# Optimization experiments

Hardware: AMD Instinct MI355X
Metric: run time of the kernel (lower is better)

Reference implementation:

```python
import jax, jax.numpy as jnp
import numpy as np

NUM_HEADS = 8
EPS = 1e-9


def setup_inputs() -> dict:
    key = jax.random.key(0)
    ks = jax.random.split(key, 5)
    B, S, D = 2, 2048, 512
    x = jax.random.normal(ks[0], (B, S, D), dtype=jnp.float32)
    Wq = jax.random.normal(ks[1], (D, D), dtype=jnp.float32) * (1.0 / np.sqrt(D))
    Wk = jax.random.normal(ks[2], (D, D), dtype=jnp.float32) * (1.0 / np.sqrt(D))
    Wv = jax.random.normal(ks[3], (D, D), dtype=jnp.float32) * (1.0 / np.sqrt(D))
    Wo = jax.random.normal(ks[4], (D, D), dtype=jnp.float32) * (1.0 / np.sqrt(D))
    gamma = jnp.ones((D,), dtype=jnp.float32)
    beta = jnp.zeros((D,), dtype=jnp.float32)
    return {"x": x, "Wq": Wq, "Wk": Wk, "Wv": Wv, "Wo": Wo, "gamma": gamma, "beta": beta}


def _layernorm(x, gamma, beta):
    mean = jnp.mean(x, axis=-1, keepdims=True)
    var = jnp.mean(jnp.square(x - mean), axis=-1, keepdims=True)
    return gamma * ((x - mean) * jax.lax.rsqrt(var + EPS)) + beta


def reference(x, Wq, Wk, Wv, Wo, gamma, beta):
    B, S, D = x.shape
    H = NUM_HEADS
    dh = D // H
    # Note: in the original, K_V=(inputs, inputs) is captured BEFORE LayerNorm,
    # so only Q is layer-normalized; K and V use the raw inputs.
    q_in = _layernorm(x, gamma, beta)
    Q = jnp.einsum('bsd,de->bse', q_in, Wq).reshape(B, S, H, dh)
    K = jnp.einsum('bsd,de->bse', x, Wk).reshape(B, S, H, dh)
    V = jnp.einsum('bsd,de->bse', x, Wv).reshape(B, S, H, dh)
    # scaled dot-product attention (bias = 0, dropout disabled since dropout=1)
    scores = jnp.einsum('bqhd,bkhd->bhqk', Q, K) / jnp.sqrt(jnp.float32(dh))
    attn = jax.nn.softmax(scores, axis=-1)
    ctx = jnp.einsum('bhqk,bkhd->bqhd', attn, V).reshape(B, S, D)
    out = jnp.einsum('bsd,de->bse', ctx, Wo) + x  # output proj + residual
    return out
```

## Files before the change

kernel.cpp:

```cpp
#include <hip/hip_runtime.h>

typedef __bf16 bf16x8 __attribute__((ext_vector_type(8)));
typedef float f32x4 __attribute__((ext_vector_type(4)));

#define SCALE_LOG2E 0.18033688011112042f

__device__ __forceinline__ float bf2f(unsigned int u) { return __uint_as_float(u << 16); }
__device__ __forceinline__ unsigned short f2bfu(float f) {
    union { __bf16 h; unsigned short u; } v;
    v.h = (__bf16)f;
    return v.u;
}
__device__ __forceinline__ unsigned int pk2bf(float a, float b) {
    union { __bf16 h[2]; unsigned int u; } v;
    v.h[0] = (__bf16)a; v.h[1] = (__bf16)b;
    return v.u;
}

__device__ int probe_bf16(const void* xp) {
    const unsigned short* u = (const unsigned short*)xp;
    int cnt = 0;
    for (int i = 0; i < 128; i++) {
        unsigned e = (u[i] >> 7) & 0xFFu;
        cnt += (e == 0u || (e >= 0x6Cu && e <= 0x8Au)) ? 1 : 0;
    }
    return cnt >= 120;
}

__global__ __launch_bounds__(64)
void probe_k(const void* __restrict__ x, const void* __restrict__ Wq, int* __restrict__ flags) {
    if (threadIdx.x == 0) {
        flags[0] = probe_bf16(x);
        flags[1] = probe_bf16(Wq);
    }
}

__device__ __forceinline__ void load8f(const void* p, int isb, size_t idx, float* o) {
    if (isb) {
        uint4 v = *(const uint4*)((const unsigned short*)p + idx);
        o[0] = bf2f(v.x & 0xffffu); o[1] = bf2f(v.x >> 16);
        o[2] = bf2f(v.y & 0xffffu); o[3] = bf2f(v.y >> 16);
        o[4] = bf2f(v.z & 0xffffu); o[5] = bf2f(v.z >> 16);
        o[6] = bf2f(v.w & 0xffffu); o[7] = bf2f(v.w >> 16);
    } else {
        const float* f = (const float*)p + idx;
        float4 a = *(const float4*)f;
        float4 b = *(const float4*)(f + 4);
        o[0] = a.x; o[1] = a.y; o[2] = a.z; o[3] = a.w;
        o[4] = b.x; o[5] = b.y; o[6] = b.z; o[7] = b.w;
    }
}
__device__ __forceinline__ void load2f(const void* p, int isb, size_t idx, float& a, float& b) {
    if (isb) {
        unsigned int v = *(const unsigned int*)((const unsigned short*)p + idx);
        a = bf2f(v & 0xffffu); b = bf2f(v >> 16);
    } else {
        float2 f = *(const float2*)((const float*)p + idx);
        a = f.x; b = f.y;
    }
}
__device__ __forceinline__ float load1f(const void* p, int isb, size_t idx) {
    return isb ? bf2f((unsigned int)((const unsigned short*)p)[idx]) : ((const float*)p)[idx];
}

__global__ __launch_bounds__(256)
void setup_k(const void* __restrict__ x, const void* __restrict__ Wq, const void* __restrict__ Wk,
             const void* __restrict__ Wv, const void* __restrict__ Wo,
             const void* __restrict__ gamma, const void* __restrict__ beta,
             float* __restrict__ rowstats, float* __restrict__ gf, float* __restrict__ bfv,
             unsigned short* __restrict__ WT, const int* __restrict__ flags) {
    const int t = threadIdx.x;
    const int bid = blockIdx.x;
    if (bid < 1024) {
        const int isb = flags[1];
        __shared__ float tile[32][33];
        const int which = bid >> 8, tl = bid & 255;
        const int bx = (tl & 15) * 32, by = (tl >> 4) * 32;
        const void* W = (which == 0) ? Wq : (which == 1) ? Wk : (which == 2) ? Wv : Wo;
        unsigned short* dst = WT + (size_t)which * 512 * 512;
        const int xx = t & 31, y0 = t >> 5;
#pragma unroll
        for (int i = 0; i < 4; i++) {
            int y = y0 + i * 8;
            tile[y][xx] = load1f(W, isb, (size_t)(by + y) * 512 + bx + xx);
        }
        __syncthreads();
#pragma unroll
        for (int i = 0; i < 4; i++) {
            int y = y0 + i * 8;
            dst[(size_t)(bx + y) * 512 + by + xx] = f2bfu(tile[xx][y]);
        }
        return;
    }
    const int isb = flags[0];
    if (bid >= 5120) {
        const void* src = (bid == 5120) ? gamma : beta;
        float* dst = (bid == 5120) ? gf : bfv;
        float a, b;
        load2f(src, isb, (size_t)t * 2, a, b);
        dst[t * 2] = a; dst[t * 2 + 1] = b;
        return;
    }
    const int row = bid - 1024;
    float a, b;
    load2f(x, isb, (size_t)row * 512 + t * 2, a, b);
    float s = a + b, sq = a * a + b * b;
#pragma unroll
    for (int msk = 1; msk < 64; msk <<= 1) {
        s += __shfl_xor(s, msk);
        sq += __shfl_xor(sq, msk);
    }
    __shared__ float red[8];
    if ((t & 63) == 0) { red[t >> 6] = s; red[4 + (t >> 6)] = sq; }
    __syncthreads();
    if (t == 0) {
        float S = red[0] + red[1] + red[2] + red[3];
        float SQ = red[4] + red[5] + red[6] + red[7];
        float mean = S * (1.0f / 512.0f);
        float var = SQ * (1.0f / 512.0f) - mean * mean;
        rowstats[2 * row] = mean;
        rowstats[2 * row + 1] = rsqrtf(fmaxf(var, 0.0f) + 1e-9f);
    }
}

__global__ __launch_bounds__(512)
void proj_all_k(const void* __restrict__ x, const unsigned short* __restrict__ WT,
                const float* __restrict__ rowstats, const float* __restrict__ gf,
                const float* __restrict__ bfv, unsigned short* __restrict__ Qb,
                unsigned short* __restrict__ Kb, unsigned short* __restrict__ VtF,
                const int* __restrict__ flags) {
    __shared__ unsigned short As[128 * 40];
    __shared__ unsigned short Bs[128 * 40];
    __shared__ float Gs[512], Bts[512];
    const int t = threadIdx.x;
    const int isb = flags[0];
    const int w = t >> 6, lane = t & 63;
    const int quad = lane >> 4, ln = lane & 15;
    const f32x4 zero = {0.f, 0.f, 0.f, 0.f};

    if (blockIdx.z == 0) {
        const int role = blockIdx.x & 1;
        const int n0 = (blockIdx.x >> 1) * 128;
        const int m0 = blockIdx.y * 128;
        const unsigned short* BT = WT + (size_t)role * 512 * 512;
        unsigned short* out = role ? Kb : Qb;
        const int wm = w & 1, wn = w >> 1;
        Gs[t] = gf[t]; Bts[t] = bfv[t];

        f32x4 acc[4][2];
#pragma unroll
        for (int i = 0; i < 4; i++)
#pragma unroll
            for (int j = 0; j < 2; j++) acc[i][j] = zero;

        for (int kt = 0; kt < 512; kt += 32) {
            __syncthreads();
            {
                int r = t >> 2, c8 = t & 3;
                size_t gidx = (size_t)(m0 + r) * 512 + kt + c8 * 8;
                if (isb && role == 1) {
                    *(uint4*)(&As[r * 40 + c8 * 8]) = *(const uint4*)((const unsigned short*)x + gidx);
                } else {
                    float f[8];
                    load8f(x, isb, gidx, f);
                    if (role == 0) {
                        float mean = rowstats[2 * (m0 + r)];
                        float inv = rowstats[2 * (m0 + r) + 1];
#pragma unroll
                        for (int j = 0; j < 8; j++) {
                            int k = kt + c8 * 8 + j;
                            f[j] = (f[j] - mean) * inv * Gs[k] + Bts[k];
                        }
                    }
                    unsigned int pk[4];
#pragma unroll
                    for (int j = 0; j < 4; j++) pk[j] = pk2bf(f[2 * j], f[2 * j + 1]);
                    *(uint4*)(&As[r * 40 + c8 * 8]) = make_uint4(pk[0], pk[1], pk[2], pk[3]);
                }
            }
            {
                int r = t >> 2, c8 = t & 3;
                *(uint4*)(&Bs[r * 40 + c8 * 8]) = *(const uint4*)(BT + (size_t)(n0 + r) * 512 + kt + c8 * 8);
            }
            __syncthreads();
            bf16x8 af[4], bfr[2];
#pragma unroll
            for (int i = 0; i < 4; i++)
                af[i] = *(const bf16x8*)(&As[(wm * 64 + i * 16 + ln) * 40 + quad * 8]);
#pragma unroll
            for (int j = 0; j < 2; j++)
                bfr[j] = *(const bf16x8*)(&Bs[(wn * 32 + j * 16 + ln) * 40 + quad * 8]);
#pragma unroll
            for (int i = 0; i < 4; i++)
#pragma unroll
                for (int j = 0; j < 2; j++)
                    acc[i][j] = __builtin_amdgcn_mfma_f32_16x16x32_bf16(af[i], bfr[j], acc[i][j], 0, 0, 0);
        }
#pragma unroll
        for (int i = 0; i < 4; i++)
#pragma unroll
            for (int j = 0; j < 2; j++)
#pragma unroll
                for (int r = 0; r < 4; r++) {
                    int grow = m0 + wm * 64 + i * 16 + quad * 4 + r;
                    int gcol = n0 + wn * 32 + j * 16 + ln;
                    float v = acc[i][j][r];
                    if (role == 0) v *= SCALE_LOG2E;
                    out[(size_t)grow * 512 + gcol] = f2bfu(v);
                }
    } else {
        const int m0 = blockIdx.x * 64;
        const int n0 = blockIdx.y * 128;
        const unsigned short* AW = WT + (size_t)2 * 512 * 512;
        const int wv = w & 3, wn2 = w >> 2;

        f32x4 acc[4];
#pragma unroll
        for (int j = 0; j < 4; j++) acc[j] = zero;

        for (int kt = 0; kt < 512; kt += 32) {
            __syncthreads();
            if (t < 256) {
                int r = t >> 2, c8 = t & 3;
                *(uint4*)(&As[r * 40 + c8 * 8]) = *(const uint4*)(AW + (size_t)(m0 + r) * 512 + kt + c8 * 8);
            }
            {
                int r = t >> 2, c8 = t & 3;
                size_t gidx = (size_t)(n0 + r) * 512 + kt + c8 * 8;
                if (isb) {
                    *(uint4*)(&Bs[r * 40 + c8 * 8]) = *(const uint4*)((const unsigned short*)x + gidx);
                } else {
                    float f[8];
                    load8f(x, isb, gidx, f);
                    unsigned int pk[4];
#pragma unroll
                    for (int j = 0; j < 4; j++) pk[j] = pk2bf(f[2 * j], f[2 * j + 1]);
                    *(uint4*)(&Bs[r * 40 + c8 * 8]) = make_uint4(pk[0], pk[1], pk[2], pk[3]);
                }
            }
            __syncthreads();
            bf16x8 af = *(const bf16x8*)(&As[(wv * 16 + ln) * 40 + quad * 8]);
#pragma unroll
            for (int j = 0; j < 4; j++) {
                bf16x8 bfr = *(const bf16x8*)(&Bs[(wn2 * 64 + j * 16 + ln) * 40 + quad * 8]);
                acc[j] = __builtin_amdgcn_mfma_f32_16x16x32_bf16(af, bfr, acc[j], 0, 0, 0);
            }
        }
#pragma unroll
        for (int j = 0; j < 4; j++)
#pragma unroll
            for (int r = 0; r < 4; r++) {
                int grow = m0 + wv * 16 + quad * 4 + r;
                int gcol = n0 + wn2 * 64 + j * 16 + ln;
                VtF[(size_t)grow * 4096 + gcol] = f2bfu(acc[j][r]);
            }
    }
}

__global__ __launch_bounds__(1024, 1)
void attn_m_k(const unsigned short* __restrict__ Qb, const unsigned short* __restrict__ Kb,
              const unsigned short* __restrict__ VtF, unsigned short* __restrict__ ctx) {
    const int S = 2048, PT = 72, NT = 32;
    const int t = threadIdx.x;
    const int qb = blockIdx.x, h = blockIdx.y, b = blockIdx.z;
    const int w = t >> 6, lane = t & 63;
    const int quad = lane >> 4, ln = lane & 15;
    const int kq = w & 3, qh = w >> 2;

    __shared__ unsigned short sh[27648];
    unsigned short* const KsA = sh;
    unsigned short* const KsB = sh + 4608;
    unsigned short* const Vt0 = sh + 9216;
    unsigned short* const Vt1 = sh + 13824;
    unsigned short* const Vt2 = sh + 18432;
    unsigned short* const Vt3 = sh + 23040;
    unsigned short* const Qs  = sh + 18432;

    const size_t baseQ  = (size_t)(b * S + qb * 128) * 512 + h * 64;
    const size_t baseK  = (size_t)(b * S) * 512 + h * 64;
    const size_t baseVt = (size_t)(h * 64) * 4096 + (size_t)b * S;

    const int c8 = t & 7;
    const int r64 = (t & 511) >> 3;
    const int stoff = r64 * PT + c8 * 8;

    const int kfo0 = (kq * 16 + ln) * PT + quad * 8;
    const int vto  = ln * PT + kq * 16 + quad * 4;

    const unsigned short* const gK = Kb + baseK + (size_t)r64 * 512 + c8 * 8;
    const unsigned short* const gV = VtF + baseVt + (size_t)r64 * 4096 + c8 * 8;

    uint4 sa, sb;
    if (t < 512) { sa = *(const uint4*)(gK); sb = *(const uint4*)(gK + 32768); }
    else         { sa = *(const uint4*)(gV); sb = *(const uint4*)(gV + 64); }

    {
        const int rQ = t >> 3;
        *(uint4*)(&Qs[rQ * PT + c8 * 8]) = *(const uint4*)(Qb + baseQ + (size_t)rQ * 512 + c8 * 8);
    }
    __syncthreads();
    bf16x8 qf[2][2];
#pragma unroll
    for (int s2 = 0; s2 < 2; s2++)
#pragma unroll
        for (int i = 0; i < 2; i++)
            qf[s2][i] = *(const bf16x8*)(&Qs[(qh * 32 + s2 * 16 + ln) * PT + quad * 8 + 32 * i]);

    f32x4 acc[2][4];
    const f32x4 zero = {0.f, 0.f, 0.f, 0.f};
#pragma unroll
    for (int s2 = 0; s2 < 2; s2++)
#pragma unroll
        for (int j = 0; j < 4; j++) acc[s2][j] = zero;
    float lsum0 = 0.f, lsum1 = 0.f;

#define STAGE(KS, VT, R)                                                    \
    {                                                                       \
        if (t < 512) *(uint4*)(&KS[stoff]) = R;                             \
        else         *(uint4*)(&VT[stoff]) = R;                             \
    }
#define PRELOAD(R, kt)                                                      \
    if ((kt) < NT) {                                                        \
        if (t < 512) R = *(const uint4*)(gK + (size_t)(kt) * 32768);        \
        else         R = *(const uint4*)(gV + (size_t)(kt) * 64);           \
    }
#define QK_EXP(KS, U00, U01, U10, U11)                                      \
    {                                                                       \
        bf16x8 kf0 = *(const bf16x8*)(&KS[kfo0]);                           \
        bf16x8 kf1 = *(const bf16x8*)(&KS[kfo0 + 32]);                      \
        f32x4 sc0 = zero, sc1 = zero;                                       \
        sc0 = __builtin_amdgcn_mfma_f32_16x16x32_bf16(kf0, qf[0][0], sc0, 0, 0, 0); \
        sc0 = __builtin_amdgcn_mfma_f32_16x16x32_bf16(kf1, qf[0][1], sc0, 0, 0, 0); \
        sc1 = __builtin_amdgcn_mfma_f32_16x16x32_bf16(kf0, qf[1][0], sc1, 0, 0, 0); \
        sc1 = __builtin_amdgcn_mfma_f32_16x16x32_bf16(kf1, qf[1][1], sc1, 0, 0, 0); \
        float a0 = __builtin_amdgcn_exp2f(fminf(sc0[0], 30.f));             \
        float a1 = __builtin_amdgcn_exp2f(fminf(sc0[1], 30.f));             \
        float a2 = __builtin_amdgcn_exp2f(fminf(sc0[2], 30.f));             \
        float a3 = __builtin_amdgcn_exp2f(fminf(sc0[3], 30.f));             \
        lsum0 += (a0 + a1) + (a2 + a3);                                     \
        U00 = pk2bf(a0, a1); U01 = pk2bf(a2, a3);                           \
        float b0 = __builtin_amdgcn_exp2f(fminf(sc1[0], 30.f));             \
        float b1 = __builtin_amdgcn_exp2f(fminf(sc1[1], 30.f));             \
        float b2 = __builtin_amdgcn_exp2f(fminf(sc1[2], 30.f));             \
        float b3 = __builtin_amdgcn_exp2f(fminf(sc1[3], 30.f));             \
        lsum1 += (b0 + b1) + (b2 + b3);                                     \
        U10 = pk2bf(b0, b1); U11 = pk2bf(b2, b3);                           \
    }
#define PV4(VTE, VTO)                                                       \
    {                                                                       \
        bf16x8 ap0 = __builtin_bit_cast(bf16x8, make_uint4(uA00, uA01, uB00, uB01)); \
        bf16x8 ap1 = __builtin_bit_cast(bf16x8, make_uint4(uA10, uA11, uB10, uB11)); \
        _Pragma("unroll")                                                   \
        for (int nt = 0; nt < 4; nt++) {                                    \
            uint2 ve = *(const uint2*)(&VTE[vto + nt * 16 * PT]);           \
            uint2 vo = *(const uint2*)(&VTO[vto + nt * 16 * PT]);           \
            bf16x8 vb = __builtin_bit_cast(bf16x8, make_uint4(ve.x, ve.y, vo.x, vo.y)); \
            acc[0][nt] = __builtin_amdgcn_mfma_f32_16x16x32_bf16(ap0, vb, acc[0][nt], 0, 0, 0); \
            acc[1][nt] = __builtin_amdgcn_mfma_f32_16x16x32_bf16(ap1, vb, acc[1][nt], 0, 0, 0); \
        }                                                                   \
    }

    for (int m = 0; m < 8; m++) {
        const int T = m * 4;
        unsigned int uA00, uA01, uA10, uA11, uB00, uB01, uB10, uB11;
        STAGE(KsA, Vt0, sa);
        __syncthreads();
        PRELOAD(sa, T + 2);
        QK_EXP(KsA, uA00, uA01, uA10, uA11);
        STAGE(KsB, Vt1, sb);
        __syncthreads();
        PRELOAD(sb, T + 3);
        QK_EXP(KsB, uB00, uB01, uB10, uB11);
        PV4(Vt0, Vt1);
        STAGE(KsA, Vt2, sa);
        __syncthreads();
        PRELOAD(sa, T + 4);
        QK_EXP(KsA, uA00, uA01, uA10, uA11);
        STAGE(KsB, Vt3, sb);
        __syncthreads();
        PRELOAD(sb, T + 5);
        QK_EXP(KsB, uB00, uB01, uB10, uB11);
        PV4(Vt2, Vt3);
    }
#undef STAGE
#undef PRELOAD
#undef QK_EXP
#undef PV4

    lsum0 += __shfl_xor(lsum0, 16);
    lsum0 += __shfl_xor(lsum0, 32);
    lsum1 += __shfl_xor(lsum1, 16);
    lsum1 += __shfl_xor(lsum1, 32);

    __syncthreads();
    float* scr  = (float*)sh;
    float* lred = scr + 13056;
    if (quad == 0) {
        lred[kq * 128 + qh * 32 + ln] = lsum0;
        lred[kq * 128 + qh * 32 + 16 + ln] = lsum1;
    }
#pragma unroll
    for (int rr = 0; rr < 2; rr++) {
        __syncthreads();
        if ((qh >> 1) == rr && kq != 0) {
            const int pb = (kq - 1) * 4352 + ((qh & 1) * 32 + quad * 4) * 68 + ln;
#pragma unroll
            for (int s2 = 0; s2 < 2; s2++)
#pragma unroll
                for (int nt = 0; nt < 4; nt++)
#pragma unroll
                    for (int r = 0; r < 4; r++)
                        scr[pb + (s2 * 16 + r) * 68 + nt * 16] = acc[s2][nt][r];
        }
        __syncthreads();
        if ((qh >> 1) == rr && kq == 0) {
#pragma unroll
            for (int s2 = 0; s2 < 2; s2++) {
                const size_t baseO = (size_t)(b * S + qb * 128 + qh * 32 + s2 * 16 + quad * 4) * 512 + h * 64 + ln;
#pragma unroll
                for (int r = 0; r < 4; r++) {
                    int qrow = qh * 32 + s2 * 16 + quad * 4 + r;
                    float lt = lred[qrow] + lred[128 + qrow] + lred[256 + qrow] + lred[384 + qrow];
                    float inv = 1.0f / lt;
                    int rb = ((qh & 1) * 32 + s2 * 16 + quad * 4 + r) * 68 + ln;
#pragma unroll
                    for (int nt = 0; nt < 4; nt++) {
                        float v = acc[s2][nt][r] + scr[rb + nt * 16] + scr[4352 + rb + nt * 16] + scr[8704 + rb + nt * 16];
                        ctx[baseO + (size_t)r * 512 + nt * 16] = f2bfu(v * inv);
                    }
                }
            }
        }
    }
}

__global__ __launch_bounds__(512)
void outproj_k(const unsigned short* __restrict__ ctx, const unsigned short* __restrict__ BT,
               const void* __restrict__ x, void* __restrict__ outp, const int* __restrict__ flags) {
    __shared__ unsigned short As[128 * 40];
    __shared__ unsigned short Bs[64 * 40];
    const int t = threadIdx.x;
    const int isb = flags[0];
    const int m0 = blockIdx.y * 128, n0 = blockIdx.x * 64;
    const int w = t >> 6, lane = t & 63;
    const int wm = w & 1, wn = w >> 1;
    const int quad = lane >> 4, ln = lane & 15;

    f32x4 acc[4];
    const f32x4 zero = {0.f, 0.f, 0.f, 0.f};
#pragma unroll
    for (int i = 0; i < 4; i++) acc[i] = zero;

    for (int kt = 0; kt < 512; kt += 32) {
        __syncthreads();
        {
            int r = t >> 2, c8 = t & 3;
            *(uint4*)(&As[r * 40 + c8 * 8]) = *(const uint4*)(ctx + (size_t)(m0 + r) * 512 + kt + c8 * 8);
        }
        if (t < 256) {
            int r = t >> 2, c8 = t & 3;
            *(uint4*)(&Bs[r * 40 + c8 * 8]) = *(const uint4*)(BT + (size_t)(n0 + r) * 512 + kt + c8 * 8);
        }
        __syncthreads();
        bf16x8 af[4];
#pragma unroll
        for (int i = 0; i < 4; i++)
            af[i] = *(const bf16x8*)(&As[(wm * 64 + i * 16 + ln) * 40 + quad * 8]);
        bf16x8 bfr = *(const bf16x8*)(&Bs[(wn * 16 + ln) * 40 + quad * 8]);
#pragma unroll
        for (int i = 0; i < 4; i++)
            acc[i] = __builtin_amdgcn_mfma_f32_16x16x32_bf16(af[i], bfr, acc[i], 0, 0, 0);
    }
#pragma unroll
    for (int i = 0; i < 4; i++)
#pragma unroll
        for (int r = 0; r < 4; r++) {
            int grow = m0 + wm * 64 + i * 16 + quad * 4 + r;
            int gcol = n0 + wn * 16 + ln;
            size_t idx = (size_t)grow * 512 + gcol;
            float v = acc[i][r] + load1f(x, isb, idx);
            if (isb) ((unsigned short*)outp)[idx] = f2bfu(v);
            else     ((float*)outp)[idx] = v;
        }
}

__global__ __launch_bounds__(256)
void fill_k(unsigned short* out, int n) {
    int i = blockIdx.x * 256 + threadIdx.x;
    if (i < n) out[i] = 0x4442;
}

extern "C" void kernel_launch(void* const* d_in, const int* in_sizes, int n_in,
                              void* d_out, int out_size, void* d_ws, size_t ws_size,
                              hipStream_t stream) {
    const void* x     = d_in[0];
    const void* Wq    = d_in[1];
    const void* Wk    = d_in[2];
    const void* Wv    = d_in[3];
    const void* Wo    = d_in[4];
    const void* gamma = d_in[5];
    const void* beta  = d_in[6];

    const size_t NW = 512 * 512;
    const size_t NX = 4096 * 512;
    char* w = (char*)d_ws;

    const size_t FULL_STATS_OFF = 2097152 + 3 * NX * 2;
    const size_t NEED_FULL = FULL_STATS_OFF + 32768 + 4096 + 16;

    if (ws_size < NEED_FULL) {
        fill_k<<<(out_size + 255) / 256, 256, 0, stream>>>((unsigned short*)d_out, out_size);
        return;
    }

    unsigned short* WT  = (unsigned short*)w;
    unsigned short* Qb  = (unsigned short*)(w + 2097152);
    unsigned short* Kb  = Qb + NX;
    unsigned short* VtF = Kb + NX;
    unsigned short* ctx = Qb;
    float* rowstats = (float*)(w + FULL_STATS_OFF);
    float* gf = rowstats + 8192;
    float* bfv = gf + 512;
    int* flags = (int*)(bfv + 512);

    probe_k<<<1, 64, 0, stream>>>(x, Wq, flags);
    setup_k<<<5122, 256, 0, stream>>>(x, Wq, Wk, Wv, Wo, gamma, beta, rowstats, gf, bfv, WT, flags);
    proj_all_k<<<dim3(8, 32, 2), 512, 0, stream>>>(x, WT, rowstats, gf, bfv, Qb, Kb, VtF, flags);
    attn_m_k<<<dim3(16, 8, 2), 1024, 0, stream>>>(Qb, Kb, VtF, ctx);
    outproj_k<<<dim3(8, 32), 512, 0, stream>>>(ctx, WT + 3 * NW, x, d_out, flags);
}
```

Measured before the change: 156.3 us.

## Register-prefetch next K-tile in projection GEMMs, widen K-step, retile outproj

The projection and output-projection GEMMs now load the next 64-wide K slice from global memory into registers while MFMAs run on the current slice in shared memory. The K step doubles from 32 to 64 with padded 72-element LDS rows, which halves the barrier count. LayerNorm row stats are hoisted out of the loop. The output projection switches to 64x64 tiles, doubling its grid for better occupancy, at the cost of more register pressure and less reuse per block.

```diff
diff --git a/kernel.cpp b/kernel.cpp
--- a/kernel.cpp
+++ b/kernel.cpp
@@ -35,21 +35,6 @@
     }
 }
 
-__device__ __forceinline__ void load8f(const void* p, int isb, size_t idx, float* o) {
-    if (isb) {
-        uint4 v = *(const uint4*)((const unsigned short*)p + idx);
-        o[0] = bf2f(v.x & 0xffffu); o[1] = bf2f(v.x >> 16);
-        o[2] = bf2f(v.y & 0xffffu); o[3] = bf2f(v.y >> 16);
-        o[4] = bf2f(v.z & 0xffffu); o[5] = bf2f(v.z >> 16);
-        o[6] = bf2f(v.w & 0xffffu); o[7] = bf2f(v.w >> 16);
-    } else {
-        const float* f = (const float*)p + idx;
-        float4 a = *(const float4*)f;
-        float4 b = *(const float4*)(f + 4);
-        o[0] = a.x; o[1] = a.y; o[2] = a.z; o[3] = a.w;
-        o[4] = b.x; o[5] = b.y; o[6] = b.z; o[7] = b.w;
-    }
-}
 __device__ __forceinline__ void load2f(const void* p, int isb, size_t idx, float& a, float& b) {
     if (isb) {
         unsigned int v = *(const unsigned int*)((const unsigned short*)p + idx);
@@ -61,6 +46,20 @@
 }
 __device__ __forceinline__ float load1f(const void* p, int isb, size_t idx) {
     return isb ? bf2f((unsigned int)((const unsigned short*)p)[idx]) : ((const float*)p)[idx];
+}
+
+__device__ __forceinline__ void unpack8(int isb, uint4 p0, uint4 p1, float* f) {
+    if (isb) {
+        f[0] = bf2f(p0.x & 0xffffu); f[1] = bf2f(p0.x >> 16);
+        f[2] = bf2f(p0.y & 0xffffu); f[3] = bf2f(p0.y >> 16);
+        f[4] = bf2f(p0.z & 0xffffu); f[5] = bf2f(p0.z >> 16);
+        f[6] = bf2f(p0.w & 0xffffu); f[7] = bf2f(p0.w >> 16);
+    } else {
+        f[0] = __uint_as_float(p0.x); f[1] = __uint_as_float(p0.y);
+        f[2] = __uint_as_float(p0.z); f[3] = __uint_as_float(p0.w);
+        f[4] = __uint_as_float(p1.x); f[5] = __uint_as_float(p1.y);
+        f[6] = __uint_as_float(p1.z); f[7] = __uint_as_float(p1.w);
+    }
 }
 
 __global__ __launch_bounds__(256)
@@ -129,8 +128,8 @@
                 const float* __restrict__ bfv, unsigned short* __restrict__ Qb,
                 unsigned short* __restrict__ Kb, unsigned short* __restrict__ VtF,
                 const int* __restrict__ flags) {
-    __shared__ unsigned short As[128 * 40];
-    __shared__ unsigned short Bs[128 * 40];
+    __shared__ unsigned short As[128 * 72];
+    __shared__ unsigned short Bs[128 * 72];
     __shared__ float Gs[512], Bts[512];
     const int t = threadIdx.x;
     const int isb = flags[0];
@@ -146,6 +145,13 @@
         unsigned short* out = role ? Kb : Qb;
         const int wm = w & 1, wn = w >> 1;
         Gs[t] = gf[t]; Bts[t] = bfv[t];
+        float mean[2], rinv[2];
+#pragma unroll
+        for (int i = 0; i < 2; i++) {
+            int r = (t >> 3) + i * 64;
+            mean[i] = rowstats[2 * (m0 + r)];
+            rinv[i] = rowstats[2 * (m0 + r) + 1];
+        }
 
         f32x4 acc[4][2];
 #pragma unroll
@@ -153,48 +159,66 @@
 #pragma unroll
             for (int j = 0; j < 2; j++) acc[i][j] = zero;
 
-        for (int kt = 0; kt < 512; kt += 32) {
+        uint4 pa0[2], pa1[2], pbv[2];
+#pragma unroll
+        for (int i = 0; i < 2; i++) {
+            int o = t + i * 512, r = o >> 3, c = o & 7;
+            size_t gidx = (size_t)(m0 + r) * 512 + c * 8;
+            if (isb) pa0[i] = *(const uint4*)((const unsigned short*)x + gidx);
+            else { const float* f = (const float*)x + gidx; pa0[i] = *(const uint4*)f; pa1[i] = *(const uint4*)(f + 4); }
+            pbv[i] = *(const uint4*)(BT + (size_t)(n0 + r) * 512 + c * 8);
+        }
+
+        for (int kt = 0; kt < 512; kt += 64) {
             __syncthreads();
-            {
-                int r = t >> 2, c8 = t & 3;
-                size_t gidx = (size_t)(m0 + r) * 512 + kt + c8 * 8;
+#pragma unroll
+            for (int i = 0; i < 2; i++) {
+                int o = t + i * 512, r = o >> 3, c = o & 7;
                 if (isb && role == 1) {
-                    *(uint4*)(&As[r * 40 + c8 * 8]) = *(const uint4*)((const unsigned short*)x + gidx);
+                    *(uint4*)(&As[r * 72 + c * 8]) = pa0[i];
                 } else {
                     float f[8];
-                    load8f(x, isb, gidx, f);
+                    unpack8(isb, pa0[i], pa1[i], f);
                     if (role == 0) {
-                        float mean = rowstats[2 * (m0 + r)];
-                        float inv = rowstats[2 * (m0 + r) + 1];
 #pragma unroll
                         for (int j = 0; j < 8; j++) {
-                            int k = kt + c8 * 8 + j;
-                            f[j] = (f[j] - mean) * inv * Gs[k] + Bts[k];
+                            int k = kt + c * 8 + j;
+                            f[j] = (f[j] - mean[i]) * rinv[i] * Gs[k] + Bts[k];
                         }
                     }
                     unsigned int pk[4];
 #pragma unroll
                     for (int j = 0; j < 4; j++) pk[j] = pk2bf(f[2 * j], f[2 * j + 1]);
-                    *(uint4*)(&As[r * 40 + c8 * 8]) = make_uint4(pk[0], pk[1], pk[2], pk[3]);
-                }
-            }
-            {
-                int r = t >> 2, c8 = t & 3;
-                *(uint4*)(&Bs[r * 40 + c8 * 8]) = *(const uint4*)(BT + (size_t)(n0 + r) * 512 + kt + c8 * 8);
+                    *(uint4*)(&As[r * 72 + c * 8]) = make_uint4(pk[0], pk[1], pk[2], pk[3]);
+                }
+                *(uint4*)(&Bs[r * 72 + c * 8]) = pbv[i];
             }
             __syncthreads();
-            bf16x8 af[4], bfr[2];
-#pragma unroll
-            for (int i = 0; i < 4; i++)
-                af[i] = *(const bf16x8*)(&As[(wm * 64 + i * 16 + ln) * 40 + quad * 8]);
-#pragma unroll
-            for (int j = 0; j < 2; j++)
-                bfr[j] = *(const bf16x8*)(&Bs[(wn * 32 + j * 16 + ln) * 40 + quad * 8]);
-#pragma unroll
-            for (int i = 0; i < 4; i++)
+            if (kt + 64 < 512) {
+#pragma unroll
+                for (int i = 0; i < 2; i++) {
+                    int o = t + i * 512, r = o >> 3, c = o & 7;
+                    size_t gidx = (size_t)(m0 + r) * 512 + (kt + 64) + c * 8;
+                    if (isb) pa0[i] = *(const uint4*)((const unsigned short*)x + gidx);
+                    else { const float* f = (const float*)x + gidx; pa0[i] = *(const uint4*)f; pa1[i] = *(const uint4*)(f + 4); }
+                    pbv[i] = *(const uint4*)(BT + (size_t)(n0 + r) * 512 + (kt + 64) + c * 8);
+                }
+            }
+#pragma unroll
+            for (int ks = 0; ks < 2; ks++) {
+                bf16x8 af[4], bfr[2];
+#pragma unroll
+                for (int i = 0; i < 4; i++)
+                    af[i] = *(const bf16x8*)(&As[(wm * 64 + i * 16 + ln) * 72 + ks * 32 + quad * 8]);
 #pragma unroll
                 for (int j = 0; j < 2; j++)
-                    acc[i][j] = __builtin_amdgcn_mfma_f32_16x16x32_bf16(af[i], bfr[j], acc[i][j], 0, 0, 0);
+                    bfr[j] = *(const bf16x8*)(&Bs[(wn * 32 + j * 16 + ln) * 72 + ks * 32 + quad * 8]);
+#pragma unroll
+                for (int i = 0; i < 4; i++)
+#pragma unroll
+                    for (int j = 0; j < 2; j++)
+                        acc[i][j] = __builtin_amdgcn_mfma_f32_16x16x32_bf16(af[i], bfr[j], acc[i][j], 0, 0, 0);
+            }
         }
 #pragma unroll
         for (int i = 0; i < 4; i++)
@@ -218,32 +242,59 @@
 #pragma unroll
         for (int j = 0; j < 4; j++) acc[j] = zero;
 
-        for (int kt = 0; kt < 512; kt += 32) {
+        uint4 pa, pb0[2], pb1[2];
+        {
+            int r = t >> 3, c = t & 7;
+            pa = *(const uint4*)(AW + (size_t)(m0 + r) * 512 + c * 8);
+        }
+#pragma unroll
+        for (int i = 0; i < 2; i++) {
+            int o = t + i * 512, r = o >> 3, c = o & 7;
+            size_t gidx = (size_t)(n0 + r) * 512 + c * 8;
+            if (isb) pb0[i] = *(const uint4*)((const unsigned short*)x + gidx);
+            else { const float* f = (const float*)x + gidx; pb0[i] = *(const uint4*)f; pb1[i] = *(const uint4*)(f + 4); }
+        }
+
+        for (int kt = 0; kt < 512; kt += 64) {
             __syncthreads();
-            if (t < 256) {
-                int r = t >> 2, c8 = t & 3;
-                *(uint4*)(&As[r * 40 + c8 * 8]) = *(const uint4*)(AW + (size_t)(m0 + r) * 512 + kt + c8 * 8);
-            }
             {
-                int r = t >> 2, c8 = t & 3;
-                size_t gidx = (size_t)(n0 + r) * 512 + kt + c8 * 8;
+                int r = t >> 3, c = t & 7;
+                *(uint4*)(&As[r * 72 + c * 8]) = pa;
+            }
+#pragma unroll
+            for (int i = 0; i < 2; i++) {
+                int o = t + i * 512, r = o >> 3, c = o & 7;
                 if (isb) {
-                    *(uint4*)(&Bs[r * 40 + c8 * 8]) = *(const uint4*)((const unsigned short*)x + gidx);
+                    *(uint4*)(&Bs[r * 72 + c * 8]) = pb0[i];
                 } else {
                     float f[8];
-                    load8f(x, isb, gidx, f);
+                    unpack8(0, pb0[i], pb1[i], f);
                     unsigned int pk[4];
 #pragma unroll
                     for (int j = 0; j < 4; j++) pk[j] = pk2bf(f[2 * j], f[2 * j + 1]);
-                    *(uint4*)(&Bs[r * 40 + c8 * 8]) = make_uint4(pk[0], pk[1], pk[2], pk[3]);
+                    *(uint4*)(&Bs[r * 72 + c * 8]) = make_uint4(pk[0], pk[1], pk[2], pk[3]);
                 }
             }
             __syncthreads();
-            bf16x8 af = *(const bf16x8*)(&As[(wv * 16 + ln) * 40 + quad * 8]);
-#pragma unroll
-            for (int j = 0; j < 4; j++) {
-                bf16x8 bfr = *(const bf16x8*)(&Bs[(wn2 * 64 + j * 16 + ln) * 40 + quad * 8]);
-                acc[j] = __builtin_amdgcn_mfma_f32_16x16x32_bf16(af, bfr, acc[j], 0, 0, 0);
+            if (kt + 64 < 512) {
+                int r = t >> 3, c = t & 7;
+                pa = *(const uint4*)(AW + (size_t)(m0 + r) * 512 + (kt + 64) + c * 8);
+#pragma unroll
+                for (int i = 0; i < 2; i++) {
+                    int o = t + i * 512, r2 = o >> 3, c2 = o & 7;
+                    size_t gidx = (size_t)(n0 + r2) * 512 + (kt + 64) + c2 * 8;
+                    if (isb) pb0[i] = *(const uint4*)((const unsigned short*)x + gidx);
+                    else { const float* f = (const float*)x + gidx; pb0[i] = *(const uint4*)f; pb1[i] = *(const uint4*)(f + 4); }
+                }
+            }
+#pragma unroll
+            for (int ks = 0; ks < 2; ks++) {
+                bf16x8 af = *(const bf16x8*)(&As[(wv * 16 + ln) * 72 + ks * 32 + quad * 8]);
+#pragma unroll
+                for (int j = 0; j < 4; j++) {
+                    bf16x8 bfr = *(const bf16x8*)(&Bs[(wn2 * 64 + j * 16 + ln) * 72 + ks * 32 + quad * 8]);
+                    acc[j] = __builtin_amdgcn_mfma_f32_16x16x32_bf16(af, bfr, acc[j], 0, 0, 0);
+                }
             }
         }
 #pragma unroll
@@ -437,48 +488,65 @@
 __global__ __launch_bounds__(512)
 void outproj_k(const unsigned short* __restrict__ ctx, const unsigned short* __restrict__ BT,
                const void* __restrict__ x, void* __restrict__ outp, const int* __restrict__ flags) {
-    __shared__ unsigned short As[128 * 40];
-    __shared__ unsigned short Bs[64 * 40];
+    __shared__ unsigned short As[64 * 72];
+    __shared__ unsigned short Bs[64 * 72];
     const int t = threadIdx.x;
     const int isb = flags[0];
-    const int m0 = blockIdx.y * 128, n0 = blockIdx.x * 64;
+    const int m0 = blockIdx.y * 64, n0 = blockIdx.x * 64;
     const int w = t >> 6, lane = t & 63;
-    const int wm = w & 1, wn = w >> 1;
+    const int wm = w & 3, wn = w >> 2;
     const int quad = lane >> 4, ln = lane & 15;
 
-    f32x4 acc[4];
+    const int isA = t < 256;
+    int ro[2], co[2];
+#pragma unroll
+    for (int i = 0; i < 2; i++) {
+        int o = (t & 255) + i * 256;
+        ro[i] = o >> 3; co[i] = o & 7;
+    }
+    const unsigned short* gb = isA ? ctx : BT;
+    const int rbase = isA ? m0 : n0;
+
+    f32x4 acc[2];
     const f32x4 zero = {0.f, 0.f, 0.f, 0.f};
-#pragma unroll
-    for (int i = 0; i < 4; i++) acc[i] = zero;
-
-    for (int kt = 0; kt < 512; kt += 32) {
-        __syncthreads();
-        {
-            int r = t >> 2, c8 = t & 3;
-            *(uint4*)(&As[r * 40 + c8 * 8]) = *(const uint4*)(ctx + (size_t)(m0 + r) * 512 + kt + c8 * 8);
-        }
-        if (t < 256) {
-            int r = t >> 2, c8 = t & 3;
-            *(uint4*)(&Bs[r * 40 + c8 * 8]) = *(const uint4*)(BT + (size_t)(n0 + r) * 512 + kt + c8 * 8);
-        }
-        __syncthreads();
-        bf16x8 af[4];
-#pragma unroll
-        for (int i = 0; i < 4; i++)
-            af[i] = *(const bf16x8*)(&As[(wm * 64 + i * 16 + ln) * 40 + quad * 8]);
-        bf16x8 bfr = *(const bf16x8*)(&Bs[(wn * 16 + ln) * 40 + quad * 8]);
-#pragma unroll
-        for (int i = 0; i < 4; i++)
-            acc[i] = __builtin_amdgcn_mfma_f32_16x16x32_bf16(af[i], bfr, acc[i], 0, 0, 0);
-    }
-#pragma unroll
-    for (int i = 0; i < 4; i++)
+    acc[0] = zero; acc[1] = zero;
+
+    uint4 ps[2];
+#pragma unroll
+    for (int i = 0; i < 2; i++)
+        ps[i] = *(const uint4*)(gb + (size_t)(rbase + ro[i]) * 512 + co[i] * 8);
+
+    for (int kt = 0; kt < 512; kt += 64) {
+        __syncthreads();
+#pragma unroll
+        for (int i = 0; i < 2; i++) {
+            if (isA) *(uint4*)(&As[ro[i] * 72 + co[i] * 8]) = ps[i];
+            else     *(uint4*)(&Bs[ro[i] * 72 + co[i] * 8]) = ps[i];
+        }
+        __syncthreads();
+        if (kt + 64 < 512) {
+#pragma unroll
+            for (int i = 0; i < 2; i++)
+                ps[i] = *(const uint4*)(gb + (size_t)(rbase + ro[i]) * 512 + (kt + 64) + co[i] * 8);
+        }
+#pragma unroll
+        for (int ks = 0; ks < 2; ks++) {
+            bf16x8 af = *(const bf16x8*)(&As[(wm * 16 + ln) * 72 + ks * 32 + quad * 8]);
+#pragma unroll
+            for (int j = 0; j < 2; j++) {
+                bf16x8 bfr = *(const bf16x8*)(&Bs[(wn * 32 + j * 16 + ln) * 72 + ks * 32 + quad * 8]);
+                acc[j] = __builtin_amdgcn_mfma_f32_16x16x32_bf16(af, bfr, acc[j], 0, 0, 0);
+            }
+        }
+    }
+#pragma unroll
+    for (int j = 0; j < 2; j++)
 #pragma unroll
         for (int r = 0; r < 4; r++) {
-            int grow = m0 + wm * 64 + i * 16 + quad * 4 + r;
-            int gcol = n0 + wn * 16 + ln;
+            int grow = m0 + wm * 16 + quad * 4 + r;
+            int gcol = n0 + wn * 32 + j * 16 + ln;
             size_t idx = (size_t)grow * 512 + gcol;
-            float v = acc[i][r] + load1f(x, isb, idx);
+            float v = acc[j][r] + load1f(x, isb, idx);
             if (isb) ((unsigned short*)outp)[idx] = f2bfu(v);
             else     ((float*)outp)[idx] = v;
         }
@@ -527,5 +595,5 @@
     setup_k<<<5122, 256, 0, stream>>>(x, Wq, Wk, Wv, Wo, gamma, beta, rowstats, gf, bfv, WT, flags);
     proj_all_k<<<dim3(8, 32, 2), 512, 0, stream>>>(x, WT, rowstats, gf, bfv, Qb, Kb, VtF, flags);
     attn_m_k<<<dim3(16, 8, 2), 1024, 0, stream>>>(Qb, Kb, VtF, ctx);
-    outproj_k<<<dim3(8, 32), 512, 0, stream>>>(ctx, WT + 3 * NW, x, d_out, flags);
-}
+    outproj_k<<<dim3(8, 64), 512, 0, stream>>>(ctx, WT + 3 * NW, x, d_out, flags);
+}
```

After: 173.7 us. +11.2%, slower.
